# Optimization experiments

Measured on AMD Instinct MI355X. Metric: run time of the kernel, lower is better.

## Reference

```python
import jax, jax.numpy as jnp
import numpy as np

B = 500000
DT = 1.0

def _first_principles_A(dt):
    A = np.eye(8, dtype=np.float32)
    for i in range(4):
        A[i, i + 4] = dt
    return jnp.asarray(A)

def setup_inputs() -> dict:
    key = jax.random.key(0)
    k1, k2 = jax.random.split(key)
    # bbox-like state: keep positions/sizes positive so Q heuristic is sensible
    x = jax.random.uniform(k1, (B, 8, 1), dtype=jnp.float32, minval=0.1, maxval=1.0)
    P = jax.random.normal(k2, (B, 8, 8), dtype=jnp.float32) * 0.1
    A = _first_principles_A(DT)  # relu/triu leave it unchanged but we apply them anyway
    sigma_p = jnp.float32(0.05)
    sigma_v = jnp.float32(0.00625)
    return {"x": x, "P": P, "A": A, "sigma_p": sigma_p, "sigma_v": sigma_v}

def reference(x, P, A, sigma_p, sigma_v):
    # get_motion_matrix: relu then triu
    Ap = jnp.triu(jax.nn.relu(A))  # (8, 8)
    # x_hat = A @ x
    x_hat = jnp.einsum('ij,bjk->bik', Ap, x)  # (B, 8, 1)
    # process-noise heuristic: diag proportional to bbox h, w (x[:,2,0], x[:,3,0])
    h = x[:, 2, 0]
    w = x[:, 3, 0]
    xp, yp = h * sigma_p, w * sigma_p
    xv, yv = h * sigma_v, w * sigma_v
    diag = jnp.stack([xp, yp, xp, yp, xv, yv, xv, yv], axis=-1)  # (B, 8)
    Q = jnp.square(diag)[:, :, None] * jnp.eye(8, dtype=x.dtype)  # (B, 8, 8) diagonal
    # P_hat = A P A^T + Q
    P_hat = jnp.einsum('ij,bjk,lk->bil', Ap, P, Ap) + Q
    return (x_hat, P_hat)
```

## Files before the change

kernel.cpp:

```cpp
#include <hip/hip_runtime.h>


__global__ __launch_bounds__(256) void kalman_predict_kernel(
    const float* __restrict__ x,
    const float* __restrict__ P,
    const float* __restrict__ A,
    const float* __restrict__ sigp_ptr,
    const float* __restrict__ sigv_ptr,
    float* __restrict__ x_hat,
    float* __restrict__ P_hat,
    int B)
{
    float ap[64];
#pragma unroll
    for (int t = 0; t < 64; ++t) {
        float a = A[t];
        a = fmaxf(a, 0.0f);
        int r = t >> 3, c = t & 7;
        if (c < r) a = 0.0f;
        ap[t] = __int_as_float(__builtin_amdgcn_readfirstlane(__float_as_int(a)));
    }
    float sigma_p = __int_as_float(__builtin_amdgcn_readfirstlane(__float_as_int(sigp_ptr[0])));
    float sigma_v = __int_as_float(__builtin_amdgcn_readfirstlane(__float_as_int(sigv_ptr[0])));

    int b = blockIdx.x * blockDim.x + threadIdx.x;
    if (b >= B) return;

    const float4* x4 = (const float4*)(x + (size_t)b * 8);
    float4 xa = x4[0], xb = x4[1];
    float xv[8] = {xa.x, xa.y, xa.z, xa.w, xb.x, xb.y, xb.z, xb.w};

    float xh[8];
#pragma unroll
    for (int i = 0; i < 8; ++i) {
        float s = 0.0f;
#pragma unroll
        for (int j = 0; j < 8; ++j) s = fmaf(ap[i * 8 + j], xv[j], s);
        xh[i] = s;
    }
    float4* xo4 = (float4*)(x_hat + (size_t)b * 8);
    xo4[0] = make_float4(xh[0], xh[1], xh[2], xh[3]);
    xo4[1] = make_float4(xh[4], xh[5], xh[6], xh[7]);

    float h = xv[2], w = xv[3];
    float xp = h * sigma_p, yp = w * sigma_p;
    float xvel = h * sigma_v, yv = w * sigma_v;
    float qd[8] = {xp * xp, yp * yp, xp * xp, yp * yp,
                   xvel * xvel, yv * yv, xvel * xvel, yv * yv};

    float p[64];
    const float4* P4 = (const float4*)(P + (size_t)b * 64);
#pragma unroll
    for (int q = 0; q < 16; ++q) {
        float4 v = P4[q];
        p[q * 4 + 0] = v.x; p[q * 4 + 1] = v.y;
        p[q * 4 + 2] = v.z; p[q * 4 + 3] = v.w;
    }

    float4* po4 = (float4*)(P_hat + (size_t)b * 64);
#pragma unroll
    for (int i = 0; i < 8; ++i) {
        float t[8];
#pragma unroll
        for (int k = 0; k < 8; ++k) {
            float s = 0.0f;
#pragma unroll
            for (int j = 0; j < 8; ++j) s = fmaf(ap[i * 8 + j], p[j * 8 + k], s);
            t[k] = s;
        }
        float o[8];
#pragma unroll
        for (int l = 0; l < 8; ++l) {
            float s = (l == i) ? qd[i] : 0.0f;
#pragma unroll
            for (int k = 0; k < 8; ++k) s = fmaf(t[k], ap[l * 8 + k], s);
            o[l] = s;
        }
        po4[i * 2 + 0] = make_float4(o[0], o[1], o[2], o[3]);
        po4[i * 2 + 1] = make_float4(o[4], o[5], o[6], o[7]);
    }
}

extern "C" void kernel_launch(void* const* d_in, const int* in_sizes, int n_in,
                              void* d_out, int out_size, void* d_ws, size_t ws_size,
                              hipStream_t stream) {
    const float* x  = (const float*)d_in[0];
    const float* P  = (const float*)d_in[1];
    const float* A  = (const float*)d_in[2];
    const float* sp = (const float*)d_in[3];
    const float* sv = (const float*)d_in[4];

    int B = in_sizes[0] / 8;
    float* x_hat = (float*)d_out;
    float* P_hat = (float*)d_out + (size_t)B * 8;

    int block = 256;
    int grid = (B + block - 1) / block;
    kalman_predict_kernel<<<grid, block, 0, stream>>>(x, P, A, sp, sv, x_hat, P_hat, B);
}
```

Baseline: 298.2 us.

## Split each Kalman element across eight threads with LDS row exchange

```diff
diff --git a/kernel.cpp b/kernel.cpp
--- a/kernel.cpp
+++ b/kernel.cpp
@@ -1,5 +1,9 @@
 #include <hip/hip_runtime.h>
 
+
+#define ROW_STRIDE 12
+#define ELEM_STRIDE 100
+#define ELEMS_PER_BLOCK 32
 
 __global__ __launch_bounds__(256) void kalman_predict_kernel(
     const float* __restrict__ x,
@@ -11,73 +15,86 @@
     float* __restrict__ P_hat,
     int B)
 {
+    __shared__ float lds_m[ELEMS_PER_BLOCK * ELEM_STRIDE];
+
     float ap[64];
 #pragma unroll
     for (int t = 0; t < 64; ++t) {
-        float a = A[t];
-        a = fmaxf(a, 0.0f);
-        int r = t >> 3, c = t & 7;
-        if (c < r) a = 0.0f;
+        float a = fmaxf(A[t], 0.0f);
+        if ((t & 7) < (t >> 3)) a = 0.0f;
         ap[t] = __int_as_float(__builtin_amdgcn_readfirstlane(__float_as_int(a)));
     }
     float sigma_p = __int_as_float(__builtin_amdgcn_readfirstlane(__float_as_int(sigp_ptr[0])));
     float sigma_v = __int_as_float(__builtin_amdgcn_readfirstlane(__float_as_int(sigv_ptr[0])));
 
-    int b = blockIdx.x * blockDim.x + threadIdx.x;
-    if (b >= B) return;
+    int tid = blockIdx.x * blockDim.x + threadIdx.x;
+    int e = tid >> 3;
+    int r = tid & 7;
+    int e_l = threadIdx.x >> 3;
 
-    const float4* x4 = (const float4*)(x + (size_t)b * 8);
-    float4 xa = x4[0], xb = x4[1];
-    float xv[8] = {xa.x, xa.y, xa.z, xa.w, xb.x, xb.y, xb.z, xb.w};
+    bool valid = (e < B);
+    int e_c = valid ? e : (B - 1);
 
-    float xh[8];
+    const float4* prow = (const float4*)(P + (size_t)e_c * 64 + r * 8);
+    float4 pa = prow[0], pb = prow[1];
+    float p[8] = {pa.x, pa.y, pa.z, pa.w, pb.x, pb.y, pb.z, pb.w};
+
+    const float4* xrow = (const float4*)(x + (size_t)e_c * 8);
+    float4 x0 = xrow[0], x1 = xrow[1];
+    float xv[8] = {x0.x, x0.y, x0.z, x0.w, x1.x, x1.y, x1.z, x1.w};
+
+    const float4* arow = (const float4*)(A + r * 8);
+    float4 a0 = arow[0], a1 = arow[1];
+    float apr[8] = {a0.x, a0.y, a0.z, a0.w, a1.x, a1.y, a1.z, a1.w};
 #pragma unroll
-    for (int i = 0; i < 8; ++i) {
+    for (int j = 0; j < 8; ++j) {
+        float v = fmaxf(apr[j], 0.0f);
+        apr[j] = (j >= r) ? v : 0.0f;
+    }
+
+    float m[8];
+#pragma unroll
+    for (int l = 0; l < 8; ++l) {
         float s = 0.0f;
 #pragma unroll
-        for (int j = 0; j < 8; ++j) s = fmaf(ap[i * 8 + j], xv[j], s);
-        xh[i] = s;
-    }
-    float4* xo4 = (float4*)(x_hat + (size_t)b * 8);
-    xo4[0] = make_float4(xh[0], xh[1], xh[2], xh[3]);
-    xo4[1] = make_float4(xh[4], xh[5], xh[6], xh[7]);
-
-    float h = xv[2], w = xv[3];
-    float xp = h * sigma_p, yp = w * sigma_p;
-    float xvel = h * sigma_v, yv = w * sigma_v;
-    float qd[8] = {xp * xp, yp * yp, xp * xp, yp * yp,
-                   xvel * xvel, yv * yv, xvel * xvel, yv * yv};
-
-    float p[64];
-    const float4* P4 = (const float4*)(P + (size_t)b * 64);
-#pragma unroll
-    for (int q = 0; q < 16; ++q) {
-        float4 v = P4[q];
-        p[q * 4 + 0] = v.x; p[q * 4 + 1] = v.y;
-        p[q * 4 + 2] = v.z; p[q * 4 + 3] = v.w;
+        for (int k = 0; k < 8; ++k) s = fmaf(ap[l * 8 + k], p[k], s);
+        m[l] = s;
     }
 
-    float4* po4 = (float4*)(P_hat + (size_t)b * 64);
+    float* slot = lds_m + e_l * ELEM_STRIDE + r * ROW_STRIDE;
+    ((float4*)slot)[0] = make_float4(m[0], m[1], m[2], m[3]);
+    ((float4*)(slot + 4))[0] = make_float4(m[4], m[5], m[6], m[7]);
+
+    __syncthreads();
+
+    float hv = (r & 1) ? xv[3] : xv[2];
+    float sig = (r < 4) ? sigma_p : sigma_v;
+    float q = hv * sig;
+    q = q * q;
+
+    float xh = 0.0f;
 #pragma unroll
-    for (int i = 0; i < 8; ++i) {
-        float t[8];
+    for (int j = 0; j < 8; ++j) xh = fmaf(apr[j], xv[j], xh);
+
+    float out[8];
 #pragma unroll
-        for (int k = 0; k < 8; ++k) {
-            float s = 0.0f;
+    for (int l = 0; l < 8; ++l) out[l] = (l == r) ? q : 0.0f;
+
+    const float* ebase = lds_m + e_l * ELEM_STRIDE;
 #pragma unroll
-            for (int j = 0; j < 8; ++j) s = fmaf(ap[i * 8 + j], p[j * 8 + k], s);
-            t[k] = s;
-        }
-        float o[8];
+    for (int j = 0; j < 8; ++j) {
+        const float4* mr = (const float4*)(ebase + j * ROW_STRIDE);
+        float4 ma = mr[0], mb = mr[1];
+        float mj[8] = {ma.x, ma.y, ma.z, ma.w, mb.x, mb.y, mb.z, mb.w};
 #pragma unroll
-        for (int l = 0; l < 8; ++l) {
-            float s = (l == i) ? qd[i] : 0.0f;
-#pragma unroll
-            for (int k = 0; k < 8; ++k) s = fmaf(t[k], ap[l * 8 + k], s);
-            o[l] = s;
-        }
-        po4[i * 2 + 0] = make_float4(o[0], o[1], o[2], o[3]);
-        po4[i * 2 + 1] = make_float4(o[4], o[5], o[6], o[7]);
+        for (int l = 0; l < 8; ++l) out[l] = fmaf(apr[j], mj[l], out[l]);
+    }
+
+    if (valid) {
+        x_hat[(size_t)e * 8 + r] = xh;
+        float4* po = (float4*)(P_hat + (size_t)e * 64 + r * 8);
+        po[0] = make_float4(out[0], out[1], out[2], out[3]);
+        po[1] = make_float4(out[4], out[5], out[6], out[7]);
     }
 }
 
@@ -94,7 +111,8 @@
     float* x_hat = (float*)d_out;
     float* P_hat = (float*)d_out + (size_t)B * 8;
 
+    int threads = B * 8;
     int block = 256;
-    int grid = (B + block - 1) / block;
+    int grid = (threads + block - 1) / block;
     kalman_predict_kernel<<<grid, block, 0, stream>>>(x, P, A, sp, sv, x_hat, P_hat, B);
 }
```

Result: faster. 251.5 us (-15.7%).
